# Kernel optimization log

Measured on AMD Instinct MI355X. Metric: run time of the kernel, lower is better.

Reference implementation:

```python
import jax, jax.numpy as jnp
import numpy as np

DIM = 1024


def setup_inputs() -> dict:
    key = jax.random.key(0)
    ks = jax.random.split(key, 10)
    B, SQ, SKV, D = 4, 2048, 2048, DIM
    s = 1.0 / np.sqrt(D)
    return {
        "query": jax.random.normal(ks[0], (B, SQ, D), dtype=jnp.float32),
        "key_value": jax.random.normal(ks[1], (B, SKV, D), dtype=jnp.float32),
        "Wq": jax.random.normal(ks[2], (D, D), dtype=jnp.float32) * s,
        "bq": jnp.zeros((D,), dtype=jnp.float32),
        "Wk": jax.random.normal(ks[3], (D, D), dtype=jnp.float32) * s,
        "bk": jnp.zeros((D,), dtype=jnp.float32),
        "Wv": jax.random.normal(ks[4], (D, D), dtype=jnp.float32) * s,
        "bv": jnp.zeros((D,), dtype=jnp.float32),
        "Wo": jax.random.normal(ks[5], (D, D), dtype=jnp.float32) * s,
        "bo": jnp.zeros((D,), dtype=jnp.float32),
    }


def reference(query, key_value, Wq, bq, Wk, bk, Wv, bv, Wo, bo):
    # Faithful to the Keras layer: NO 1/sqrt(d) scaling, single head.
    Q = jnp.einsum("bsd,de->bse", query, Wq) + bq            # [B,Sq,D]
    K = jnp.einsum("btd,de->bte", key_value, Wk) + bk        # [B,Skv,D]
    V = jnp.einsum("btd,de->bte", key_value, Wv) + bv        # [B,Skv,D]
    scores = jnp.einsum("bse,bte->bst", Q, K)                # [B,Sq,Skv]
    attn = jax.nn.softmax(scores, axis=-1)
    ctx = jnp.einsum("bst,bte->bse", attn, V)                # [B,Sq,D]
    return jnp.einsum("bse,ef->bsf", ctx, Wo) + bo
```

## Files before the change

kernel.cpp:

```cpp
#include <hip/hip_runtime.h>
#include <cstdint>

typedef unsigned short u16;
typedef _Float16 f16;
typedef __attribute__((ext_vector_type(8))) short    s8v;
typedef __attribute__((ext_vector_type(8))) _Float16 h8v;
typedef __attribute__((ext_vector_type(4))) float    f4v;

__device__ __forceinline__ float bf2f(u16 b) {
  unsigned int u = ((unsigned int)b) << 16;
  float f;
  __builtin_memcpy(&f, &u, 4);
  return f;
}
__device__ __forceinline__ u16 f2bf(float f) {
  unsigned int u;
  __builtin_memcpy(&u, &f, 4);
  u += 0x7fffu + ((u >> 16) & 1u);
  return (u16)(u >> 16);
}

__device__ __forceinline__ void glds16(const void* g, void* l) {
  __builtin_amdgcn_global_load_lds(
      (const __attribute__((address_space(1))) unsigned int*)g,
      (__attribute__((address_space(3))) unsigned int*)l, 16, 0, 0);
}

__device__ __forceinline__ void swz_xy(int& bx, int& by) {
  const int gx = gridDim.x;
  const int p = blockIdx.y * gx + blockIdx.x;
  bx = (p >> 3) % gx;
  by = (p & 7) + 8 * (p / (gx * 8));
}

#define BM 128
#define BN 128

#define STAGE8(dstA, dstB)                                                  \
  do {                                                                      \
    glds16(ga00,      (dstA) + l0);        glds16(ga01,      (dstA) + l1);  \
    glds16(ga00 + 32, (dstA) + l0 + 4096); glds16(ga01 + 32, (dstA) + l1 + 4096); \
    glds16(gb00,      (dstB) + l0);        glds16(gb01,      (dstB) + l1);  \
    glds16(gb00 + 32, (dstB) + l0 + 4096); glds16(gb01 + 32, (dstB) + l1 + 4096); \
    ga00 += 64; ga01 += 64; gb00 += 64; gb01 += 64;                         \
  } while (0)

__global__ __launch_bounds__(256)
void detect_dtype(const u16* __restrict__ q, int* __restrict__ flg)
{
  __shared__ int cbig, czero;
  if (threadIdx.x == 0) { cbig = 0; czero = 0; }
  __syncthreads();
  int b = 0, z = 0;
  for (int i = threadIdx.x; i < 4096; i += 256) {
    float v = bf2f(q[i]);
    if (!(fabsf(v) < 1e4f)) b++;
    if ((i & 1) == 0 && q[i] == 0) z++;
  }
  atomicAdd(&cbig, b);
  atomicAdd(&czero, z);
  __syncthreads();
  if (threadIdx.x == 0) flg[0] = (cbig > 64 || czero > 1600) ? 1 : 0;
}

__global__ __launch_bounds__(256)
void convert_h(const int* __restrict__ flg,
               const void* __restrict__ q, const void* __restrict__ kv,
               f16* __restrict__ qo, f16* __restrict__ kvo, long n)
{
  const void* in = blockIdx.y ? kv : q;
  f16* out = blockIdx.y ? kvo : qo;
  const long i = ((long)blockIdx.x * 256 + threadIdx.x) * 8;
  if (i >= n) return;
  h8v h;
  if (flg[0] != 0) {
    const float* p = (const float*)in + i;
    f4v f0 = *(const f4v*)p;
    f4v f1 = *(const f4v*)(p + 4);
#pragma unroll
    for (int j = 0; j < 4; ++j) {
      h[j]     = (f16)f0[j];
      h[4 + j] = (f16)f1[j];
    }
  } else {
    s8v b = *(const s8v*)((const short*)in + i);
#pragma unroll
    for (int j = 0; j < 8; ++j) h[j] = (f16)bf2f((u16)b[j]);
  }
  *(h8v*)(out + i) = h;
}

__global__ __launch_bounds__(256)
void transpose_w4(const int* __restrict__ flg,
                  const void* __restrict__ w0, const void* __restrict__ w1,
                  const void* __restrict__ w2, const void* __restrict__ w3,
                  f16* __restrict__ h0, f16* __restrict__ h1,
                  f16* __restrict__ h2, u16* __restrict__ b3, int D)
{
  __shared__ float tile[32][33];
  const int zb = blockIdx.z;
  const void* in_v = (zb == 0) ? w0 : (zb == 1) ? w1 : (zb == 2) ? w2 : w3;
  const bool i32 = (flg[0] != 0);
  const u16*   in16 = (const u16*)in_v;
  const float* in32 = (const float*)in_v;
  const int c0 = blockIdx.x * 32, r0 = blockIdx.y * 32;
  const int tx = threadIdx.x, ty = threadIdx.y;
  for (int i = ty; i < 32; i += 8) {
    const long idx = (long)(r0 + i) * D + c0 + tx;
    tile[i][tx] = i32 ? in32[idx] : bf2f(in16[idx]);
  }
  __syncthreads();
  f16* outH = (zb == 0) ? h0 : (zb == 1) ? h1 : h2;
  for (int i = ty; i < 32; i += 8) {
    const long idx = (long)(c0 + i) * D + r0 + tx;
    const float v = tile[tx][i];
    if (zb == 3) b3[idx]   = f2bf(v);
    else         outH[idx] = (f16)v;
  }
}

__global__ __launch_bounds__(256)
void gemm_proj3(const int* __restrict__ flg,
                const f16* __restrict__ Qi, const f16* __restrict__ KVi,
                const f16* __restrict__ WqT, const f16* __restrict__ WkT,
                const f16* __restrict__ WvT,
                const void* __restrict__ bq, const void* __restrict__ bk,
                const void* __restrict__ bv,
                f16* __restrict__ Qf, f16* __restrict__ Kf,
                u16* __restrict__ Vt, int M, int N, int K, int SB)
{
  __shared__ u16 As[2 * 8192];
  __shared__ u16 Bs[2 * 8192];

  const int zb = blockIdx.z;
  const f16* A = (zb == 0) ? Qi : KVi;
  const f16* B = (zb == 0) ? WqT : (zb == 1) ? WkT : WvT;
  const void* bias = (zb == 0) ? bq : (zb == 1) ? bk : bv;

  const int f_in = flg[0];
  const int tid = threadIdx.x, lane = tid & 63, wave = tid >> 6;
  const int wm = wave >> 1, wn = wave & 1;
  int bx, by;
  swz_xy(bx, by);
  const int m0 = by * BM, n0 = bx * BN;

  const int rr  = wave * 32 + (lane >> 2);
  const int cc8 = 8 * ((lane & 3) ^ ((lane >> 3) & 3));
  const f16* ga00 = A + (long)(m0 + rr) * K + cc8;
  const f16* ga01 = ga00 + 16 * (long)K;
  const f16* gb00 = B + (long)(n0 + rr) * K + cc8;
  const f16* gb01 = gb00 + 16 * (long)K;
  const int l0 = (wave * 2) * 512, l1 = l0 + 512;

  f4v acc[4][4];
#pragma unroll
  for (int i = 0; i < 4; ++i)
#pragma unroll
    for (int j = 0; j < 4; ++j) acc[i][j] = (f4v){0.f, 0.f, 0.f, 0.f};

  const int fr  = lane & 15;
  const int fks = 8 * (((lane >> 4) ^ (lane >> 1)) & 3);
  const int aoff = (wm * 64 + fr) * 32 + fks;
  const int boff = (wn * 64 + fr) * 32 + fks;

  const int nIt = K >> 6;
  STAGE8(As, Bs);
  __syncthreads();
  for (int it = 0; it < nIt; ++it) {
    const int cb = (it & 1) * 8192;
    if (it + 1 < nIt) { STAGE8(As + (8192 - cb), Bs + (8192 - cb)); }
    {
      h8v af[4], bfr[4];
#pragma unroll
      for (int mi = 0; mi < 4; ++mi) af[mi]  = *(const h8v*)&As[cb + aoff + mi * 512];
#pragma unroll
      for (int ni = 0; ni < 4; ++ni) bfr[ni] = *(const h8v*)&Bs[cb + boff + ni * 512];
#pragma unroll
      for (int mi = 0; mi < 4; ++mi)
#pragma unroll
        for (int ni = 0; ni < 4; ++ni)
          acc[mi][ni] = __builtin_amdgcn_mfma_f32_16x16x32_f16(af[mi], bfr[ni], acc[mi][ni], 0, 0, 0);
    }
    {
      h8v af[4], bfr[4];
#pragma unroll
      for (int mi = 0; mi < 4; ++mi) af[mi]  = *(const h8v*)&As[cb + 4096 + aoff + mi * 512];
#pragma unroll
      for (int ni = 0; ni < 4; ++ni) bfr[ni] = *(const h8v*)&Bs[cb + 4096 + boff + ni * 512];
#pragma unroll
      for (int mi = 0; mi < 4; ++mi)
#pragma unroll
        for (int ni = 0; ni < 4; ++ni)
          acc[mi][ni] = __builtin_amdgcn_mfma_f32_16x16x32_f16(af[mi], bfr[ni], acc[mi][ni], 0, 0, 0);
    }
    __syncthreads();
  }

  const int cr = (lane >> 4) * 4, ccl = lane & 15;
  if (zb < 2) {
    f16* out = zb ? Kf : Qf;
#pragma unroll
    for (int ni = 0; ni < 4; ++ni) {
      const int gcol = n0 + wn * 64 + ni * 16 + ccl;
      const float bvv = (f_in != 0) ? ((const float*)bias)[gcol]
                                    : bf2f(((const u16*)bias)[gcol]);
#pragma unroll
      for (int mi = 0; mi < 4; ++mi)
#pragma unroll
        for (int r = 0; r < 4; ++r) {
          const long grow = (long)(m0 + wm * 64 + mi * 16 + cr + r);
          out[grow * N + gcol] = (f16)(acc[mi][ni][r] + bvv);
        }
    }
  } else {
    u16* xw = &As[wave * 2176];
    const int b  = m0 / SB;
    const int s0 = (m0 % SB) + wm * 64;
    const long bbase = (long)b * N * SB;
#pragma unroll
    for (int h = 0; h < 2; ++h) {
#pragma unroll
      for (int nl = 0; nl < 2; ++nl) {
        const int ni = h * 2 + nl;
        const int gcol = n0 + wn * 64 + ni * 16 + ccl;
        const float bvv = (f_in != 0) ? ((const float*)bias)[gcol]
                                      : bf2f(((const u16*)bias)[gcol]);
#pragma unroll
        for (int mi = 0; mi < 4; ++mi)
#pragma unroll
          for (int r = 0; r < 4; ++r)
            xw[(mi * 16 + cr + r) * 34 + nl * 16 + ccl] = f2bf(acc[mi][ni][r] + bvv);
      }
      __syncthreads();
#pragma unroll
      for (int c = 0; c < 32; ++c) {
        const int gcol = n0 + wn * 64 + h * 32 + c;
        Vt[bbase + (long)gcol * SB + s0 + lane] = xw[lane * 34 + c];
      }
      __syncthreads();
    }
  }
}

__global__ __launch_bounds__(256)
void gemm_sc64(const f16* __restrict__ A, const f16* __restrict__ B,
               float* __restrict__ C, int M, int N, int K,
               long sA, long sB, long sC)
{
  __shared__ u16 As[2 * 8192];
  __shared__ u16 Bs[2 * 8192];

  const int tid = threadIdx.x, lane = tid & 63, wave = tid >> 6;
  const int wm = wave >> 1, wn = wave & 1;
  int bx, by;
  swz_xy(bx, by);
  const int m0 = by * BM, n0 = bx * BN;
  const long z = blockIdx.z;

  const int rr  = wave * 32 + (lane >> 2);
  const int cc8 = 8 * ((lane & 3) ^ ((lane >> 3) & 3));
  const f16* ga00 = A + (long)(m0 + rr) * K + cc8 + z * sA;
  const f16* ga01 = ga00 + 16 * (long)K;
  const f16* gb00 = B + (long)(n0 + rr) * K + cc8 + z * sB;
  const f16* gb01 = gb00 + 16 * (long)K;
  const int l0 = (wave * 2) * 512, l1 = l0 + 512;

  f4v acc[4][4];
#pragma unroll
  for (int i = 0; i < 4; ++i)
#pragma unroll
    for (int j = 0; j < 4; ++j) acc[i][j] = (f4v){0.f, 0.f, 0.f, 0.f};

  const int fr  = lane & 15;
  const int fks = 8 * (((lane >> 4) ^ (lane >> 1)) & 3);
  const int aoff = (wm * 64 + fr) * 32 + fks;
  const int boff = (wn * 64 + fr) * 32 + fks;

  const int nIt = K >> 6;
  STAGE8(As, Bs);
  __syncthreads();
  for (int it = 0; it < nIt; ++it) {
    const int cb = (it & 1) * 8192;
    if (it + 1 < nIt) { STAGE8(As + (8192 - cb), Bs + (8192 - cb)); }
    {
      h8v af[4], bfr[4];
#pragma unroll
      for (int mi = 0; mi < 4; ++mi) af[mi]  = *(const h8v*)&As[cb + aoff + mi * 512];
#pragma unroll
      for (int ni = 0; ni < 4; ++ni) bfr[ni] = *(const h8v*)&Bs[cb + boff + ni * 512];
#pragma unroll
      for (int mi = 0; mi < 4; ++mi)
#pragma unroll
        for (int ni = 0; ni < 4; ++ni)
          acc[mi][ni] = __builtin_amdgcn_mfma_f32_16x16x32_f16(af[mi], bfr[ni], acc[mi][ni], 0, 0, 0);
    }
    {
      h8v af[4], bfr[4];
#pragma unroll
      for (int mi = 0; mi < 4; ++mi) af[mi]  = *(const h8v*)&As[cb + 4096 + aoff + mi * 512];
#pragma unroll
      for (int ni = 0; ni < 4; ++ni) bfr[ni] = *(const h8v*)&Bs[cb + 4096 + boff + ni * 512];
#pragma unroll
      for (int mi = 0; mi < 4; ++mi)
#pragma unroll
        for (int ni = 0; ni < 4; ++ni)
          acc[mi][ni] = __builtin_amdgcn_mfma_f32_16x16x32_f16(af[mi], bfr[ni], acc[mi][ni], 0, 0, 0);
    }
    __syncthreads();
  }

  const int cr = (lane >> 4) * 4, ccl = lane & 15;
#pragma unroll
  for (int ni = 0; ni < 4; ++ni) {
    const int gcol = n0 + wn * 64 + ni * 16 + ccl;
#pragma unroll
    for (int mi = 0; mi < 4; ++mi)
#pragma unroll
      for (int r = 0; r < 4; ++r) {
        const long grow = (long)(m0 + wm * 64 + mi * 16 + cr + r);
        C[z * sC + grow * N + gcol] = acc[mi][ni][r];
      }
  }
}

template<bool OUT_FLAG, bool HAS_BIAS>
__global__ __launch_bounds__(256)
void gemm_bf64(const int* __restrict__ flg, const u16* __restrict__ A,
               const u16* __restrict__ Bt, const void* __restrict__ bias,
               void* __restrict__ Cv, int M, int N, int K,
               long sA, long sB, long sC)
{
  __shared__ u16 As[2 * 8192];
  __shared__ u16 Bs[2 * 8192];

  const int f_in = flg[0];
  const int tid = threadIdx.x, lane = tid & 63, wave = tid >> 6;
  const int wm = wave >> 1, wn = wave & 1;
  int bx, by;
  swz_xy(bx, by);
  const int m0 = by * BM, n0 = bx * BN;
  const long z = blockIdx.z;

  const int rr  = wave * 32 + (lane >> 2);
  const int cc8 = 8 * ((lane & 3) ^ ((lane >> 3) & 3));
  const u16* ga00 = A + (long)(m0 + rr) * K + cc8 + z * sA;
  const u16* ga01 = ga00 + 16 * (long)K;
  const u16* gb00 = Bt + (long)(n0 + rr) * K + cc8 + z * sB;
  const u16* gb01 = gb00 + 16 * (long)K;
  const int l0 = (wave * 2) * 512, l1 = l0 + 512;

  f4v acc[4][4];
#pragma unroll
  for (int i = 0; i < 4; ++i)
#pragma unroll
    for (int j = 0; j < 4; ++j) acc[i][j] = (f4v){0.f, 0.f, 0.f, 0.f};

  const int fr  = lane & 15;
  const int fks = 8 * (((lane >> 4) ^ (lane >> 1)) & 3);
  const int aoff = (wm * 64 + fr) * 32 + fks;
  const int boff = (wn * 64 + fr) * 32 + fks;

  const int nIt = K >> 6;
  STAGE8(As, Bs);
  __syncthreads();
  for (int it = 0; it < nIt; ++it) {
    const int cb = (it & 1) * 8192;
    if (it + 1 < nIt) { STAGE8(As + (8192 - cb), Bs + (8192 - cb)); }
    {
      s8v af[4], bfr[4];
#pragma unroll
      for (int mi = 0; mi < 4; ++mi) af[mi]  = *(const s8v*)&As[cb + aoff + mi * 512];
#pragma unroll
      for (int ni = 0; ni < 4; ++ni) bfr[ni] = *(const s8v*)&Bs[cb + boff + ni * 512];
#pragma unroll
      for (int mi = 0; mi < 4; ++mi)
#pragma unroll
        for (int ni = 0; ni < 4; ++ni)
          acc[mi][ni] = __builtin_amdgcn_mfma_f32_16x16x32_bf16(af[mi], bfr[ni], acc[mi][ni], 0, 0, 0);
    }
    {
      s8v af[4], bfr[4];
#pragma unroll
      for (int mi = 0; mi < 4; ++mi) af[mi]  = *(const s8v*)&As[cb + 4096 + aoff + mi * 512];
#pragma unroll
      for (int ni = 0; ni < 4; ++ni) bfr[ni] = *(const s8v*)&Bs[cb + 4096 + boff + ni * 512];
#pragma unroll
      for (int mi = 0; mi < 4; ++mi)
#pragma unroll
        for (int ni = 0; ni < 4; ++ni)
          acc[mi][ni] = __builtin_amdgcn_mfma_f32_16x16x32_bf16(af[mi], bfr[ni], acc[mi][ni], 0, 0, 0);
    }
    __syncthreads();
  }

  const int cr = (lane >> 4) * 4, ccl = lane & 15;
  const bool o32 = OUT_FLAG && (f_in != 0);
#pragma unroll
  for (int ni = 0; ni < 4; ++ni) {
    const int gcol = n0 + wn * 64 + ni * 16 + ccl;
    float bvv = 0.f;
    if (HAS_BIAS)
      bvv = (f_in != 0) ? ((const float*)bias)[gcol] : bf2f(((const u16*)bias)[gcol]);
#pragma unroll
    for (int mi = 0; mi < 4; ++mi)
#pragma unroll
      for (int r = 0; r < 4; ++r) {
        const long grow = (long)(m0 + wm * 64 + mi * 16 + cr + r);
        const float val = acc[mi][ni][r] + bvv;
        const long idx = z * sC + grow * N + gcol;
        if (o32) ((float*)Cv)[idx] = val;
        else     ((u16*)Cv)[idx]   = f2bf(val);
      }
  }
}

__global__ __launch_bounds__(256)
void softmax_rows_bf(const float* __restrict__ S, u16* __restrict__ P, int N)
{
  const float* row = S + (long)blockIdx.x * N;
  u16* prow = P + (long)blockIdx.x * N;
  const int t = threadIdx.x;
  f4v v0 = *(const f4v*)(row + t * 8);
  f4v v1 = *(const f4v*)(row + t * 8 + 4);

  float m = v0[0];
#pragma unroll
  for (int j = 1; j < 4; ++j) m = fmaxf(m, v0[j]);
#pragma unroll
  for (int j = 0; j < 4; ++j) m = fmaxf(m, v1[j]);
  for (int off = 32; off > 0; off >>= 1) m = fmaxf(m, __shfl_down(m, off, 64));

  __shared__ float redm[4], reds[4];
  if ((t & 63) == 0) redm[t >> 6] = m;
  __syncthreads();
  m = fmaxf(fmaxf(redm[0], redm[1]), fmaxf(redm[2], redm[3]));

  float s = 0.f;
#pragma unroll
  for (int j = 0; j < 4; ++j) { v0[j] = __expf(v0[j] - m); s += v0[j]; }
#pragma unroll
  for (int j = 0; j < 4; ++j) { v1[j] = __expf(v1[j] - m); s += v1[j]; }
  for (int off = 32; off > 0; off >>= 1) s += __shfl_down(s, off, 64);
  if ((t & 63) == 0) reds[t >> 6] = s;
  __syncthreads();
  s = reds[0] + reds[1] + reds[2] + reds[3];

  const float inv = 1.f / s;
  s8v o;
#pragma unroll
  for (int j = 0; j < 4; ++j) {
    o[j]     = (short)f2bf(v0[j] * inv);
    o[4 + j] = (short)f2bf(v1[j] * inv);
  }
  *(s8v*)(prow + t * 8) = o;
}

extern "C" void kernel_launch(void* const* d_in, const int* in_sizes, int n_in,
                              void* d_out, int out_size, void* d_ws, size_t ws_size,
                              hipStream_t stream)
{
  const void* query = d_in[0];
  const void* kv    = d_in[1];
  const void* Wq    = d_in[2];
  const void* bq    = d_in[3];
  const void* Wk    = d_in[4];
  const void* bk    = d_in[5];
  const void* Wv    = d_in[6];
  const void* bv    = d_in[7];
  const void* Wo    = d_in[8];
  const void* bo    = d_in[9];

  const int Bn = 4, S = 2048, D = 1024;
  const int MS = Bn * S;
  const size_t KBu = 1024, MBu = 1024 * 1024;
  const long nTok = (long)MS * D;

  char* ws = (char*)d_ws;
  int*  flg  = (int*)(ws);
  f16*  Qi   = (f16*)(ws + 64 * KBu);
  f16*  KVi  = (f16*)(ws + 64 * KBu + 16 * MBu);
  char* rW   = ws + 64 * KBu + 32 * MBu;
  f16*  WqT  = (f16*)(rW);
  f16*  WkT  = (f16*)(rW + 2 * MBu);
  f16*  WvT  = (f16*)(rW + 4 * MBu);
  u16*  WoT  = (u16*)(rW + 6 * MBu);
  char* rQK  = rW + 8 * MBu;
  f16*  Qf   = (f16*)(rQK);
  f16*  Kf   = (f16*)(rQK + 16 * MBu);
  u16*  attn = (u16*)(rQK);
  float* Sc  = (float*)(rQK + 32 * MBu);
  char* rV   = rQK + 96 * MBu;
  u16*  Vt   = (u16*)(rV);
  u16*  Cx   = (u16*)(rV + 16 * MBu);

  detect_dtype<<<1, 256, 0, stream>>>((const u16*)query, flg);

  convert_h<<<dim3((unsigned)(nTok / 2048), 2), 256, 0, stream>>>(
      flg, query, kv, Qi, KVi, nTok);

  dim3 tb(32, 8);
  transpose_w4<<<dim3(32, 32, 4), tb, 0, stream>>>(
      flg, Wq, Wk, Wv, Wo, WqT, WkT, WvT, WoT, D);

  gemm_proj3<<<dim3(D / BN, MS / BM, 3), 256, 0, stream>>>(
      flg, Qi, KVi, WqT, WkT, WvT, bq, bk, bv, Qf, Kf, Vt, MS, D, D, S);

  gemm_sc64<<<dim3(S / BN, S / BM, Bn), 256, 0, stream>>>(
      Qf, Kf, Sc, S, S, D, (long)S * D, (long)S * D, (long)S * S);
  softmax_rows_bf<<<dim3(Bn * S), 256, 0, stream>>>(Sc, attn, S);
  gemm_bf64<false, false><<<dim3(D / BN, S / BM, Bn), 256, 0, stream>>>(
      flg, attn, Vt, nullptr, Cx, S, D, S, (long)S * S, (long)D * S, (long)S * D);

  gemm_bf64<true, true><<<dim3(D / BN, MS / BM, 1), 256, 0, stream>>>(
      flg, Cx, WoT, bo, d_out, MS, D, D, 0L, 0L, 0L);
}
```

Baseline: 343.1 us.

## Enlarge GEMM tiles to 256 with 8 waves and a 4-slot LDS pipeline

Replaces the double-buffered 128x128 GEMM kernels with 256x256 (and 256x128) tiles run by 512 threads. They share a templated pipeK routine that keeps a 4-slot ring of K=32 sub-tiles in LDS, prefetching two steps ahead. It uses explicit vmcnt waits and raw s_barrier instead of __syncthreads, and raises wave priority around the MFMA block. Larger tiles are meant to improve operand reuse and cut global traffic, and the deeper pipeline should hide load latency better. The cost is more LDS and registers (8x4 accumulators), lower occupancy, and fewer blocks on small grids such as the projection GEMMs.

```diff
diff --git a/kernel.cpp b/kernel.cpp
--- a/kernel.cpp
+++ b/kernel.cpp
@@ -1,5 +1,6 @@
 #include <hip/hip_runtime.h>
 #include <cstdint>
+#include <type_traits>
 
 typedef unsigned short u16;
 typedef _Float16 f16;
@@ -33,17 +34,55 @@
   by = (p & 7) + 8 * (p / (gx * 8));
 }
 
-#define BM 128
-#define BN 128
-
-#define STAGE8(dstA, dstB)                                                  \
-  do {                                                                      \
-    glds16(ga00,      (dstA) + l0);        glds16(ga01,      (dstA) + l1);  \
-    glds16(ga00 + 32, (dstA) + l0 + 4096); glds16(ga01 + 32, (dstA) + l1 + 4096); \
-    glds16(gb00,      (dstB) + l0);        glds16(gb01,      (dstB) + l1);  \
-    glds16(gb00 + 32, (dstB) + l0 + 4096); glds16(gb01 + 32, (dstB) + l1 + 4096); \
-    ga00 += 64; ga01 += 64; gb00 += 64; gb01 += 64;                         \
-  } while (0)
+template<bool BF, int MI, int NB, int SLOTU>
+__device__ __forceinline__ void pipeK(u16* Ls,
+    const u16* ga0, const u16* ga1, const u16* gb0, const u16* gb1,
+    const int stA, const int stB, const int aoff, const int boff,
+    const int nSub, f4v (&acc)[MI][4])
+{
+  using FV = typename std::conditional<BF, s8v, h8v>::type;
+  auto stage = [&](int st) {
+    glds16(ga0, Ls + st + stA);
+    glds16(ga1, Ls + st + stA + 512);
+    glds16(gb0, Ls + st + stB);
+    if constexpr (NB == 2) { glds16(gb1, Ls + st + stB + 512); gb1 += 32; }
+    ga0 += 32; ga1 += 32; gb0 += 32;
+  };
+  stage(0);
+  stage(SLOTU);
+  if constexpr (NB == 2) asm volatile("s_waitcnt vmcnt(4)" ::: "memory");
+  else                   asm volatile("s_waitcnt vmcnt(3)" ::: "memory");
+  __builtin_amdgcn_s_barrier();
+
+  for (int s = 0; s < nSub; ++s) {
+    const int sl = (s & 3) * SLOTU;
+    FV af[MI], bv[4];
+#pragma unroll
+    for (int mi = 0; mi < MI; ++mi) af[mi] = *(const FV*)&Ls[sl + aoff + mi * 512];
+#pragma unroll
+    for (int ni = 0; ni < 4; ++ni)  bv[ni] = *(const FV*)&Ls[sl + boff + ni * 512];
+    const bool more = (s + 2 < nSub);
+    if (more) stage(((s + 2) & 3) * SLOTU);
+    __builtin_amdgcn_s_setprio(1);
+#pragma unroll
+    for (int mi = 0; mi < MI; ++mi)
+#pragma unroll
+      for (int ni = 0; ni < 4; ++ni) {
+        if constexpr (BF)
+          acc[mi][ni] = __builtin_amdgcn_mfma_f32_16x16x32_bf16(af[mi], bv[ni], acc[mi][ni], 0, 0, 0);
+        else
+          acc[mi][ni] = __builtin_amdgcn_mfma_f32_16x16x32_f16(af[mi], bv[ni], acc[mi][ni], 0, 0, 0);
+      }
+    __builtin_amdgcn_s_setprio(0);
+    if (more) {
+      if constexpr (NB == 2) asm volatile("s_waitcnt vmcnt(4)" ::: "memory");
+      else                   asm volatile("s_waitcnt vmcnt(3)" ::: "memory");
+    } else {
+      asm volatile("s_waitcnt vmcnt(0)" ::: "memory");
+    }
+    __builtin_amdgcn_s_barrier();
+  }
+}
 
 __global__ __launch_bounds__(256)
 void detect_dtype(const u16* __restrict__ q, int* __restrict__ flg)
@@ -119,7 +158,7 @@
   }
 }
 
-__global__ __launch_bounds__(256)
+__global__ __launch_bounds__(512)
 void gemm_proj3(const int* __restrict__ flg,
                 const f16* __restrict__ Qi, const f16* __restrict__ KVi,
                 const f16* __restrict__ WqT, const f16* __restrict__ WkT,
@@ -129,72 +168,39 @@
                 f16* __restrict__ Qf, f16* __restrict__ Kf,
                 u16* __restrict__ Vt, int M, int N, int K, int SB)
 {
-  __shared__ u16 As[2 * 8192];
-  __shared__ u16 Bs[2 * 8192];
-
+  __shared__ u16 Ls[65536];
   const int zb = blockIdx.z;
-  const f16* A = (zb == 0) ? Qi : KVi;
-  const f16* B = (zb == 0) ? WqT : (zb == 1) ? WkT : WvT;
+  const u16* A = (const u16*)((zb == 0) ? Qi : KVi);
+  const u16* B = (const u16*)((zb == 0) ? WqT : (zb == 1) ? WkT : WvT);
   const void* bias = (zb == 0) ? bq : (zb == 1) ? bk : bv;
-
-  const int f_in = flg[0];
+  int f_in = flg[0];
+  asm volatile("" : "+v"(f_in));
+
   const int tid = threadIdx.x, lane = tid & 63, wave = tid >> 6;
-  const int wm = wave >> 1, wn = wave & 1;
-  int bx, by;
-  swz_xy(bx, by);
-  const int m0 = by * BM, n0 = bx * BN;
+  const int wm = wave >> 2, wn = wave & 3;
+  int bx, by; swz_xy(bx, by);
+  const int m0 = by * 256, n0 = bx * 256;
 
   const int rr  = wave * 32 + (lane >> 2);
   const int cc8 = 8 * ((lane & 3) ^ ((lane >> 3) & 3));
-  const f16* ga00 = A + (long)(m0 + rr) * K + cc8;
-  const f16* ga01 = ga00 + 16 * (long)K;
-  const f16* gb00 = B + (long)(n0 + rr) * K + cc8;
-  const f16* gb01 = gb00 + 16 * (long)K;
-  const int l0 = (wave * 2) * 512, l1 = l0 + 512;
-
-  f4v acc[4][4];
-#pragma unroll
-  for (int i = 0; i < 4; ++i)
-#pragma unroll
-    for (int j = 0; j < 4; ++j) acc[i][j] = (f4v){0.f, 0.f, 0.f, 0.f};
+  const u16* ga0 = A + (long)(m0 + rr) * K + cc8;
+  const u16* ga1 = ga0 + 16 * (long)K;
+  const u16* gb0 = B + (long)(n0 + rr) * K + cc8;
+  const u16* gb1 = gb0 + 16 * (long)K;
+  const int stA = wave * 1024, stB = 8192 + wave * 1024;
 
   const int fr  = lane & 15;
   const int fks = 8 * (((lane >> 4) ^ (lane >> 1)) & 3);
-  const int aoff = (wm * 64 + fr) * 32 + fks;
-  const int boff = (wn * 64 + fr) * 32 + fks;
-
-  const int nIt = K >> 6;
-  STAGE8(As, Bs);
-  __syncthreads();
-  for (int it = 0; it < nIt; ++it) {
-    const int cb = (it & 1) * 8192;
-    if (it + 1 < nIt) { STAGE8(As + (8192 - cb), Bs + (8192 - cb)); }
-    {
-      h8v af[4], bfr[4];
-#pragma unroll
-      for (int mi = 0; mi < 4; ++mi) af[mi]  = *(const h8v*)&As[cb + aoff + mi * 512];
-#pragma unroll
-      for (int ni = 0; ni < 4; ++ni) bfr[ni] = *(const h8v*)&Bs[cb + boff + ni * 512];
-#pragma unroll
-      for (int mi = 0; mi < 4; ++mi)
-#pragma unroll
-        for (int ni = 0; ni < 4; ++ni)
-          acc[mi][ni] = __builtin_amdgcn_mfma_f32_16x16x32_f16(af[mi], bfr[ni], acc[mi][ni], 0, 0, 0);
-    }
-    {
-      h8v af[4], bfr[4];
-#pragma unroll
-      for (int mi = 0; mi < 4; ++mi) af[mi]  = *(const h8v*)&As[cb + 4096 + aoff + mi * 512];
-#pragma unroll
-      for (int ni = 0; ni < 4; ++ni) bfr[ni] = *(const h8v*)&Bs[cb + 4096 + boff + ni * 512];
-#pragma unroll
-      for (int mi = 0; mi < 4; ++mi)
-#pragma unroll
-        for (int ni = 0; ni < 4; ++ni)
-          acc[mi][ni] = __builtin_amdgcn_mfma_f32_16x16x32_f16(af[mi], bfr[ni], acc[mi][ni], 0, 0, 0);
-    }
-    __syncthreads();
-  }
+  const int aoff = (wm * 128 + fr) * 32 + fks;
+  const int boff = 8192 + (wn * 64 + fr) * 32 + fks;
+
+  f4v acc[8][4];
+#pragma unroll
+  for (int i = 0; i < 8; ++i)
+#pragma unroll
+    for (int j = 0; j < 4; ++j) acc[i][j] = (f4v){0.f, 0.f, 0.f, 0.f};
+
+  pipeK<false, 8, 2, 16384>(Ls, ga0, ga1, gb0, gb1, stA, stB, aoff, boff, K >> 5, acc);
 
   const int cr = (lane >> 4) * 4, ccl = lane & 15;
   if (zb < 2) {
@@ -205,149 +211,127 @@
       const float bvv = (f_in != 0) ? ((const float*)bias)[gcol]
                                     : bf2f(((const u16*)bias)[gcol]);
 #pragma unroll
-      for (int mi = 0; mi < 4; ++mi)
+      for (int mi = 0; mi < 8; ++mi)
 #pragma unroll
         for (int r = 0; r < 4; ++r) {
-          const long grow = (long)(m0 + wm * 64 + mi * 16 + cr + r);
+          const long grow = (long)(m0 + wm * 128 + mi * 16 + cr + r);
           out[grow * N + gcol] = (f16)(acc[mi][ni][r] + bvv);
         }
     }
   } else {
-    u16* xw = &As[wave * 2176];
-    const int b  = m0 / SB;
-    const int s0 = (m0 % SB) + wm * 64;
-    const long bbase = (long)b * N * SB;
-#pragma unroll
-    for (int h = 0; h < 2; ++h) {
-#pragma unroll
-      for (int nl = 0; nl < 2; ++nl) {
-        const int ni = h * 2 + nl;
-        const int gcol = n0 + wn * 64 + ni * 16 + ccl;
-        const float bvv = (f_in != 0) ? ((const float*)bias)[gcol]
-                                      : bf2f(((const u16*)bias)[gcol]);
-#pragma unroll
-        for (int mi = 0; mi < 4; ++mi)
-#pragma unroll
-          for (int r = 0; r < 4; ++r)
-            xw[(mi * 16 + cr + r) * 34 + nl * 16 + ccl] = f2bf(acc[mi][ni][r] + bvv);
+    u16* xw = &Ls[wave * 2176];
+    const int b   = m0 / SB;
+    const int s0w = (m0 % SB) + wm * 128;
+    const long bbase = (long)b * (long)N * SB;
+    __syncthreads();
+#pragma unroll
+    for (int sh = 0; sh < 2; ++sh) {
+#pragma unroll
+      for (int dh = 0; dh < 2; ++dh) {
+#pragma unroll
+        for (int nl = 0; nl < 2; ++nl) {
+          const int ni = dh * 2 + nl;
+          const int gcol = n0 + wn * 64 + ni * 16 + ccl;
+          const float bvv = (f_in != 0) ? ((const float*)bias)[gcol]
+                                        : bf2f(((const u16*)bias)[gcol]);
+#pragma unroll
+          for (int ml = 0; ml < 4; ++ml)
+#pragma unroll
+            for (int r = 0; r < 4; ++r)
+              xw[(ml * 16 + cr + r) * 34 + nl * 16 + ccl] =
+                  f2bf(acc[sh * 4 + ml][ni][r] + bvv);
+        }
+        __syncthreads();
+#pragma unroll
+        for (int c = 0; c < 32; ++c) {
+          const int gd = n0 + wn * 64 + dh * 32 + c;
+          Vt[bbase + (long)gd * SB + s0w + sh * 64 + lane] = xw[lane * 34 + c];
+        }
+        __syncthreads();
       }
-      __syncthreads();
-#pragma unroll
-      for (int c = 0; c < 32; ++c) {
-        const int gcol = n0 + wn * 64 + h * 32 + c;
-        Vt[bbase + (long)gcol * SB + s0 + lane] = xw[lane * 34 + c];
-      }
-      __syncthreads();
     }
   }
 }
 
-__global__ __launch_bounds__(256)
-void gemm_sc64(const f16* __restrict__ A, const f16* __restrict__ B,
-               float* __restrict__ C, int M, int N, int K,
-               long sA, long sB, long sC)
-{
-  __shared__ u16 As[2 * 8192];
-  __shared__ u16 Bs[2 * 8192];
+__global__ __launch_bounds__(512)
+void gemm_sc(const f16* __restrict__ A_, const f16* __restrict__ B_,
+             float* __restrict__ C, int M, int N, int K,
+             long sA, long sB, long sC)
+{
+  __shared__ u16 Ls[65536];
+  const long z = blockIdx.z;
+  const u16* A = (const u16*)A_ + z * sA;
+  const u16* B = (const u16*)B_ + z * sB;
+
+  const int tid = threadIdx.x, lane = tid & 63, wave = tid >> 6;
+  const int wm = wave >> 2, wn = wave & 3;
+  int bx, by; swz_xy(bx, by);
+  const int m0 = by * 256, n0 = bx * 256;
+
+  const int rr  = wave * 32 + (lane >> 2);
+  const int cc8 = 8 * ((lane & 3) ^ ((lane >> 3) & 3));
+  const u16* ga0 = A + (long)(m0 + rr) * K + cc8;
+  const u16* ga1 = ga0 + 16 * (long)K;
+  const u16* gb0 = B + (long)(n0 + rr) * K + cc8;
+  const u16* gb1 = gb0 + 16 * (long)K;
+  const int stA = wave * 1024, stB = 8192 + wave * 1024;
+
+  const int fr  = lane & 15;
+  const int fks = 8 * (((lane >> 4) ^ (lane >> 1)) & 3);
+  const int aoff = (wm * 128 + fr) * 32 + fks;
+  const int boff = 8192 + (wn * 64 + fr) * 32 + fks;
+
+  f4v acc[8][4];
+#pragma unroll
+  for (int i = 0; i < 8; ++i)
+#pragma unroll
+    for (int j = 0; j < 4; ++j) acc[i][j] = (f4v){0.f, 0.f, 0.f, 0.f};
+
+  pipeK<false, 8, 2, 16384>(Ls, ga0, ga1, gb0, gb1, stA, stB, aoff, boff, K >> 5, acc);
+
+  const int cr = (lane >> 4) * 4, ccl = lane & 15;
+  float* Cz = C + z * sC;
+#pragma unroll
+  for (int ni = 0; ni < 4; ++ni) {
+    const int gcol = n0 + wn * 64 + ni * 16 + ccl;
+#pragma unroll
+    for (int mi = 0; mi < 8; ++mi)
+#pragma unroll
+      for (int r = 0; r < 4; ++r)
+        Cz[(long)(m0 + wm * 128 + mi * 16 + cr + r) * N + gcol] = acc[mi][ni][r];
+  }
+}
+
+template<bool OUT_FLAG, bool HAS_BIAS>
+__global__ __launch_bounds__(512)
+void gemm_bf(const int* __restrict__ flg, const u16* __restrict__ A_,
+             const u16* __restrict__ Bt, const void* __restrict__ bias,
+             void* __restrict__ Cv, int M, int N, int K,
+             long sA, long sB, long sC)
+{
+  __shared__ u16 Ls[49152];
+  int f_in = flg[0];
+  asm volatile("" : "+v"(f_in));
 
   const int tid = threadIdx.x, lane = tid & 63, wave = tid >> 6;
   const int wm = wave >> 1, wn = wave & 1;
-  int bx, by;
-  swz_xy(bx, by);
-  const int m0 = by * BM, n0 = bx * BN;
+  int bx, by; swz_xy(bx, by);
+  const int m0 = by * 256, n0 = bx * 128;
   const long z = blockIdx.z;
+  const u16* A = A_ + z * sA;
+  const u16* B = Bt + z * sB;
 
   const int rr  = wave * 32 + (lane >> 2);
   const int cc8 = 8 * ((lane & 3) ^ ((lane >> 3) & 3));
-  const f16* ga00 = A + (long)(m0 + rr) * K + cc8 + z * sA;
-  const f16* ga01 = ga00 + 16 * (long)K;
-  const f16* gb00 = B + (long)(n0 + rr) * K + cc8 + z * sB;
-  const f16* gb01 = gb00 + 16 * (long)K;
-  const int l0 = (wave * 2) * 512, l1 = l0 + 512;
-
-  f4v acc[4][4];
-#pragma unroll
-  for (int i = 0; i < 4; ++i)
-#pragma unroll
-    for (int j = 0; j < 4; ++j) acc[i][j] = (f4v){0.f, 0.f, 0.f, 0.f};
+  const u16* ga0 = A + (long)(m0 + rr) * K + cc8;
+  const u16* ga1 = ga0 + 16 * (long)K;
+  const u16* gb0 = B + (long)(n0 + wave * 16 + (lane >> 2)) * K + cc8;
+  const int stA = wave * 1024, stB = 8192 + wave * 512;
 
   const int fr  = lane & 15;
   const int fks = 8 * (((lane >> 4) ^ (lane >> 1)) & 3);
   const int aoff = (wm * 64 + fr) * 32 + fks;
-  const int boff = (wn * 64 + fr) * 32 + fks;
-
-  const int nIt = K >> 6;
-  STAGE8(As, Bs);
-  __syncthreads();
-  for (int it = 0; it < nIt; ++it) {
-    const int cb = (it & 1) * 8192;
-    if (it + 1 < nIt) { STAGE8(As + (8192 - cb), Bs + (8192 - cb)); }
-    {
-      h8v af[4], bfr[4];
-#pragma unroll
-      for (int mi = 0; mi < 4; ++mi) af[mi]  = *(const h8v*)&As[cb + aoff + mi * 512];
-#pragma unroll
-      for (int ni = 0; ni < 4; ++ni) bfr[ni] = *(const h8v*)&Bs[cb + boff + ni * 512];
-#pragma unroll
-      for (int mi = 0; mi < 4; ++mi)
-#pragma unroll
-        for (int ni = 0; ni < 4; ++ni)
-          acc[mi][ni] = __builtin_amdgcn_mfma_f32_16x16x32_f16(af[mi], bfr[ni], acc[mi][ni], 0, 0, 0);
-    }
-    {
-      h8v af[4], bfr[4];
-#pragma unroll
-      for (int mi = 0; mi < 4; ++mi) af[mi]  = *(const h8v*)&As[cb + 4096 + aoff + mi * 512];
-#pragma unroll
-      for (int ni = 0; ni < 4; ++ni) bfr[ni] = *(const h8v*)&Bs[cb + 4096 + boff + ni * 512];
-#pragma unroll
-      for (int mi = 0; mi < 4; ++mi)
-#pragma unroll
-        for (int ni = 0; ni < 4; ++ni)
-          acc[mi][ni] = __builtin_amdgcn_mfma_f32_16x16x32_f16(af[mi], bfr[ni], acc[mi][ni], 0, 0, 0);
-    }
-    __syncthreads();
-  }
-
-  const int cr = (lane >> 4) * 4, ccl = lane & 15;
-#pragma unroll
-  for (int ni = 0; ni < 4; ++ni) {
-    const int gcol = n0 + wn * 64 + ni * 16 + ccl;
-#pragma unroll
-    for (int mi = 0; mi < 4; ++mi)
-#pragma unroll
-      for (int r = 0; r < 4; ++r) {
-        const long grow = (long)(m0 + wm * 64 + mi * 16 + cr + r);
-        C[z * sC + grow * N + gcol] = acc[mi][ni][r];
-      }
-  }
-}
-
-template<bool OUT_FLAG, bool HAS_BIAS>
-__global__ __launch_bounds__(256)
-void gemm_bf64(const int* __restrict__ flg, const u16* __restrict__ A,
-               const u16* __restrict__ Bt, const void* __restrict__ bias,
-               void* __restrict__ Cv, int M, int N, int K,
-               long sA, long sB, long sC)
-{
-  __shared__ u16 As[2 * 8192];
-  __shared__ u16 Bs[2 * 8192];
-
-  const int f_in = flg[0];
-  const int tid = threadIdx.x, lane = tid & 63, wave = tid >> 6;
-  const int wm = wave >> 1, wn = wave & 1;
-  int bx, by;
-  swz_xy(bx, by);
-  const int m0 = by * BM, n0 = bx * BN;
-  const long z = blockIdx.z;
-
-  const int rr  = wave * 32 + (lane >> 2);
-  const int cc8 = 8 * ((lane & 3) ^ ((lane >> 3) & 3));
-  const u16* ga00 = A + (long)(m0 + rr) * K + cc8 + z * sA;
-  const u16* ga01 = ga00 + 16 * (long)K;
-  const u16* gb00 = Bt + (long)(n0 + rr) * K + cc8 + z * sB;
-  const u16* gb01 = gb00 + 16 * (long)K;
-  const int l0 = (wave * 2) * 512, l1 = l0 + 512;
+  const int boff = 8192 + (wn * 64 + fr) * 32 + fks;
 
   f4v acc[4][4];
 #pragma unroll
@@ -355,43 +339,7 @@
 #pragma unroll
     for (int j = 0; j < 4; ++j) acc[i][j] = (f4v){0.f, 0.f, 0.f, 0.f};
 
-  const int fr  = lane & 15;
-  const int fks = 8 * (((lane >> 4) ^ (lane >> 1)) & 3);
-  const int aoff = (wm * 64 + fr) * 32 + fks;
-  const int boff = (wn * 64 + fr) * 32 + fks;
-
-  const int nIt = K >> 6;
-  STAGE8(As, Bs);
-  __syncthreads();
-  for (int it = 0; it < nIt; ++it) {
-    const int cb = (it & 1) * 8192;
-    if (it + 1 < nIt) { STAGE8(As + (8192 - cb), Bs + (8192 - cb)); }
-    {
-      s8v af[4], bfr[4];
-#pragma unroll
-      for (int mi = 0; mi < 4; ++mi) af[mi]  = *(const s8v*)&As[cb + aoff + mi * 512];
-#pragma unroll
-      for (int ni = 0; ni < 4; ++ni) bfr[ni] = *(const s8v*)&Bs[cb + boff + ni * 512];
-#pragma unroll
-      for (int mi = 0; mi < 4; ++mi)
-#pragma unroll
-        for (int ni = 0; ni < 4; ++ni)
-          acc[mi][ni] = __builtin_amdgcn_mfma_f32_16x16x32_bf16(af[mi], bfr[ni], acc[mi][ni], 0, 0, 0);
-    }
-    {
-      s8v af[4], bfr[4];
-#pragma unroll
-      for (int mi = 0; mi < 4; ++mi) af[mi]  = *(const s8v*)&As[cb + 4096 + aoff + mi * 512];
-#pragma unroll
-      for (int ni = 0; ni < 4; ++ni) bfr[ni] = *(const s8v*)&Bs[cb + 4096 + boff + ni * 512];
-#pragma unroll
-      for (int mi = 0; mi < 4; ++mi)
-#pragma unroll
-        for (int ni = 0; ni < 4; ++ni)
-          acc[mi][ni] = __builtin_amdgcn_mfma_f32_16x16x32_bf16(af[mi], bfr[ni], acc[mi][ni], 0, 0, 0);
-    }
-    __syncthreads();
-  }
+  pipeK<true, 4, 1, 12288>(Ls, ga0, ga1, gb0, gb0, stA, stB, aoff, boff, K >> 5, acc);
 
   const int cr = (lane >> 4) * 4, ccl = lane & 15;
   const bool o32 = OUT_FLAG && (f_in != 0);
@@ -502,15 +450,15 @@
   transpose_w4<<<dim3(32, 32, 4), tb, 0, stream>>>(
       flg, Wq, Wk, Wv, Wo, WqT, WkT, WvT, WoT, D);
 
-  gemm_proj3<<<dim3(D / BN, MS / BM, 3), 256, 0, stream>>>(
+  gemm_proj3<<<dim3(D / 256, MS / 256, 3), 512, 0, stream>>>(
       flg, Qi, KVi, WqT, WkT, WvT, bq, bk, bv, Qf, Kf, Vt, MS, D, D, S);
 
-  gemm_sc64<<<dim3(S / BN, S / BM, Bn), 256, 0, stream>>>(
+  gemm_sc<<<dim3(S / 256, S / 256, Bn), 512, 0, stream>>>(
       Qf, Kf, Sc, S, S, D, (long)S * D, (long)S * D, (long)S * S);
   softmax_rows_bf<<<dim3(Bn * S), 256, 0, stream>>>(Sc, attn, S);
-  gemm_bf64<false, false><<<dim3(D / BN, S / BM, Bn), 256, 0, stream>>>(
+  gemm_bf<false, false><<<dim3(D / 128, S / 256, Bn), 512, 0, stream>>>(
       flg, attn, Vt, nullptr, Cx, S, D, S, (long)S * S, (long)D * S, (long)S * D);
 
-  gemm_bf64<true, true><<<dim3(D / BN, MS / BM, 1), 256, 0, stream>>>(
+  gemm_bf<true, true><<<dim3(D / 128, MS / 256, 1), 512, 0, stream>>>(
       flg, Cx, WoT, bo, d_out, MS, D, D, 0L, 0L, 0L);
 }
```

Result: slower. 354.1 us (+3.2%).
